# Kernel tuning notes

Measured on AMD Instinct MI355X. Metric: run time of the kernel, lower is better.

Reference implementation:

```python
import jax, jax.numpy as jnp
import numpy as np

RADIUS = 4
SIGMA_I = 10.0
SIGMA_X = 4.0
NUM_CLASSES = 8
PAD = RADIUS - 1          # 3, ConstantPad3d(radius-1, eps)
WIN = 2 * PAD + 1         # 7x7x7 window
EPS = float(np.finfo(np.float64).eps)


def _dist_flat():
    # spatial gaussian, zero outside the ball x^2+y^2+z^2 < radius^2
    r = np.arange(1 - RADIUS, RADIUS)
    xx, yy, zz = np.meshgrid(r, r, r, indexing='ij')
    d2 = (xx ** 2 + yy ** 2 + zz ** 2).astype(np.float32)
    dist = np.where(d2 < RADIUS ** 2, np.exp(-d2 / SIGMA_X ** 2), 0.0).astype(np.float32)
    return jnp.asarray(dist.reshape(-1))  # flattened x-major, matches i = x*49 + y*7 + z


def setup_inputs() -> dict:
    key = jax.random.key(0)
    k1, k2 = jax.random.split(key)
    batch = jax.random.normal(k1, (4, 1, 32, 32, 32), dtype=jnp.float32)
    preds = jax.random.uniform(k2, (4, 8, 32, 32, 32), dtype=jnp.float32)
    return {"batch": batch, "preds": preds}


def reference(batch, preds):
    B, _, D, H, W = batch.shape
    K = preds.shape[1]
    pad_cfg = ((0, 0), (0, 0), (PAD, PAD), (PAD, PAD), (PAD, PAD))
    pb = jnp.pad(batch, pad_cfg, constant_values=EPS)
    pp = jnp.pad(preds, pad_cfg, constant_values=EPS)
    dist_flat = _dist_flat()
    inv_sI2 = jnp.float32(1.0 / (SIGMA_I ** 2))

    def step(carry, i):
        numer, sumw = carry
        x = i // (WIN * WIN)
        y = (i // WIN) % WIN
        z = i % WIN
        sb = jax.lax.dynamic_slice(pb, (0, 0, x, y, z), (B, 1, D, H, W))
        sp = jax.lax.dynamic_slice(pp, (0, 0, x, y, z), (B, K, D, H, W))
        # affinity = intensity gaussian * spatial gaussian for this offset
        aff = jnp.exp(-jnp.square(batch - sb) * inv_sI2) * dist_flat[i]
        return (numer + aff * sp, sumw + aff), None

    init = (jnp.zeros((B, K, D, H, W), batch.dtype),
            jnp.zeros((B, 1, D, H, W), batch.dtype))
    (numer, sumw), _ = jax.lax.scan(step, init, jnp.arange(WIN ** 3))

    assocA = jnp.sum(numer * preds, axis=(2, 3, 4))  # (B, K)
    assocV = jnp.sum(sumw * preds, axis=(2, 3, 4))   # (B, K)
    return NUM_CLASSES - jnp.sum(assocA / assocV, axis=-1)  # (B,)
```

## Files before the change

### kernel.cpp

```cpp
#include <hip/hip_runtime.h>
#include <hip/hip_fp16.h>


#define EPS_F 2.220446049250313e-16f

constexpr int TD = 4, TH = 8, TW = 8;
constexpr int HDh = 7, HHh = 14, HWh = 14;
constexpr int SYB = 17;
constexpr int SXB = HHh * SYB;
constexpr int NB  = 6 * SXB + 13 * SYB + 13 + 1;
constexpr int NT = 512;
constexpr int NBLK = 512;
constexpr int NTASK = HDh * HHh * 4;

#define EX0 1.0f
#define EX1 0.93941306281347578611f
#define EX4 0.77880078307140486825f
#define EX9 0.56978282473092302544f

#define K1F (-0.014426950408889634f)
#define K2F (-0.09016844005556021f)

struct Ent { int off; float lw; };
struct Tab { Ent e[64]; int n; };

constexpr Tab make_tab(int half) {
    Tab t{};
    t.n = 0;
    for (int dxq = 0; dxq < 4; ++dxq)
        for (int dyi = 0; dyi < 7; ++dyi)
            for (int dzi = 0; dzi < 7; ++dzi) {
                int dy = dyi - 3, dz = dzi - 3;
                if (dxq == 0) {
                    if (dy < 0) continue;
                    if (dy == 0 && dz <= 0) continue;
                }
                int c2 = dxq * dxq + dy * dy + dz * dz;
                if (c2 >= 16) continue;
                if (((dyi + dzi) & 1) != half) continue;
                t.e[t.n].off = dxq * SXB + dy * SYB + dz;
                t.e[t.n].lw  = (float)c2 * K2F;
                ++t.n;
            }
    return t;
}
constexpr Tab TAB0 = make_tab(0);
constexpr Tab TAB1 = make_tab(1);

__device__ __forceinline__ unsigned pack2(float a, float b) {
    return (unsigned)__half_as_ushort(__float2half(a)) |
           ((unsigned)__half_as_ushort(__float2half(b)) << 16);
}

template <int HALF>
__device__ __forceinline__ void accum_pairs(const float* __restrict__ sB,
                                            const uint4* __restrict__ sPk,
                                            int vown, float b_own,
                                            float acc[9]) {
    constexpr Tab T = HALF ? TAB1 : TAB0;
    constexpr int N = HALF ? TAB1.n : TAB0.n;
    constexpr int N4 = (N / 4) * 4;

#pragma unroll
    for (int i = 0; i < N4; i += 4) {
        float sb[4];
        uint4 pk[4];
#pragma unroll
        for (int j = 0; j < 4; ++j) {
            const int nv = vown + T.e[i + j].off;
            sb[j] = sB[nv];
            pk[j] = sPk[nv];
        }
#pragma unroll
        for (int j = 0; j < 4; ++j) {
            const float d = b_own - sb[j];
            const float aff =
                __builtin_amdgcn_exp2f(__builtin_fmaf(d * d, K1F, T.e[i + j].lw));
            acc[8] += aff;
            __half2 h[4];
            __builtin_memcpy(h, &pk[j], 16);
            acc[0] = __builtin_fmaf(aff, __half2float(__low2half(h[0])),  acc[0]);
            acc[1] = __builtin_fmaf(aff, __half2float(__high2half(h[0])), acc[1]);
            acc[2] = __builtin_fmaf(aff, __half2float(__low2half(h[1])),  acc[2]);
            acc[3] = __builtin_fmaf(aff, __half2float(__high2half(h[1])), acc[3]);
            acc[4] = __builtin_fmaf(aff, __half2float(__low2half(h[2])),  acc[4]);
            acc[5] = __builtin_fmaf(aff, __half2float(__high2half(h[2])), acc[5]);
            acc[6] = __builtin_fmaf(aff, __half2float(__low2half(h[3])),  acc[6]);
            acc[7] = __builtin_fmaf(aff, __half2float(__high2half(h[3])), acc[7]);
        }
    }
#pragma unroll
    for (int i = N4; i < N; ++i) {
        const int nv = vown + T.e[i].off;
        const float sb = sB[nv];
        const uint4 pk = sPk[nv];
        const float d = b_own - sb;
        const float aff =
            __builtin_amdgcn_exp2f(__builtin_fmaf(d * d, K1F, T.e[i].lw));
        acc[8] += aff;
        __half2 h[4];
        __builtin_memcpy(h, &pk, 16);
        acc[0] = __builtin_fmaf(aff, __half2float(__low2half(h[0])),  acc[0]);
        acc[1] = __builtin_fmaf(aff, __half2float(__high2half(h[0])), acc[1]);
        acc[2] = __builtin_fmaf(aff, __half2float(__low2half(h[1])),  acc[2]);
        acc[3] = __builtin_fmaf(aff, __half2float(__high2half(h[1])), acc[3]);
        acc[4] = __builtin_fmaf(aff, __half2float(__low2half(h[2])),  acc[4]);
        acc[5] = __builtin_fmaf(aff, __half2float(__high2half(h[2])), acc[5]);
        acc[6] = __builtin_fmaf(aff, __half2float(__low2half(h[3])),  acc[6]);
        acc[7] = __builtin_fmaf(aff, __half2float(__high2half(h[3])), acc[7]);
    }
}

__global__ __launch_bounds__(NT, 4)
void softncuts_main(const float* __restrict__ batch,
                    const float* __restrict__ preds,
                    float* __restrict__ partials) {
    __shared__ float sB[NB];
    __shared__ uint4 sPk[NB];
    __shared__ float sRed[8][16];

    const int bid  = blockIdx.x;
    const int bb   = bid >> 7;
    const int tile = bid & 127;
    const int tw = tile & 3;
    const int th = (tile >> 2) & 3;
    const int td = tile >> 4;
    const int d0 = td * TD, h0 = th * TH, w0 = tw * TW;

    const int tid  = threadIdx.x;
    const int half = tid >> 8;
    const int vtid = tid & 255;
    const int lw = vtid & 7;
    const int lh = (vtid >> 3) & 7;
    const int ld = vtid >> 6;

    const float* bbase = batch + (size_t)bb * 32768;
    const float* pbase = preds + (size_t)bb * 8 * 32768;

    if (tid < NTASK) {
        const int t   = tid;
        const int c   = t & 3;
        const int row = t >> 2;
        const int hh  = row % HHh;
        const int hd  = row / HHh;
        const int gd  = d0 + hd;
        const int gh  = h0 + hh - 3;
        const int gw0 = w0 - 4 + c * 4;
        const int hwb = c * 4 - 1;
        const bool fast = (gd < 32) & ((unsigned)gh < 32u) & (gw0 >= 0) & (gw0 + 3 < 32);
        if (fast) {
            const int sidx = (gd * 32 + gh) * 32 + gw0;
            float4 pv[9];
            pv[0] = *(const float4*)(bbase + sidx);
#pragma unroll
            for (int k = 0; k < 8; ++k)
                pv[k + 1] = *(const float4*)(pbase + sidx + k * 32768);
#pragma unroll
            for (int e = 0; e < 4; ++e) {
                const int hw = hwb + e;
                if (hw < 0 || hw >= HWh) continue;
                const int f = hd * SXB + hh * SYB + hw;
                sB[f] = ((const float*)&pv[0])[e];
                unsigned u[4];
#pragma unroll
                for (int k = 0; k < 4; ++k)
                    u[k] = pack2(((const float*)&pv[2 * k + 1])[e],
                                 ((const float*)&pv[2 * k + 2])[e]);
                sPk[f] = make_uint4(u[0], u[1], u[2], u[3]);
            }
        } else {
#pragma unroll
            for (int e = 0; e < 4; ++e) {
                const int hw = hwb + e;
                if (hw < 0 || hw >= HWh) continue;
                const int gw = gw0 + e;
                const bool in = (gd < 32) & ((unsigned)gh < 32u) & ((unsigned)gw < 32u);
                const int sidx = (gd * 32 + gh) * 32 + gw;
                const int f = hd * SXB + hh * SYB + hw;
                sB[f] = in ? bbase[sidx] : EPS_F;
                unsigned u[4];
#pragma unroll
                for (int k = 0; k < 4; ++k)
                    u[k] = pack2(in ? pbase[sidx + (2 * k) * 32768]     : 0.f,
                                 in ? pbase[sidx + (2 * k + 1) * 32768] : 0.f);
                sPk[f] = make_uint4(u[0], u[1], u[2], u[3]);
            }
        }
    }
    __syncthreads();

    const int gdo = d0 + ld, gho = h0 + lh, gwo = w0 + lw;
    const int sidx_own = (gdo * 32 + gho) * 32 + gwo;
    const float b_own = bbase[sidx_own];
    float q[8];
#pragma unroll
    for (int k = 0; k < 8; ++k) q[k] = pbase[sidx_own + k * 32768];

    const int vown = ld * SXB + (lh + 3) * SYB + (lw + 3);

    float acc[9];
#pragma unroll
    for (int i = 0; i < 9; ++i) acc[i] = 0.f;

    if (half == 0) accum_pairs<0>(sB, sPk, vown, b_own, acc);
    else           accum_pairs<1>(sB, sPk, vown, b_own, acc);

    float S = 0.f;
    const bool border = (d0 < 3) | (h0 < 3) | (h0 + TH > 29) | (w0 < 3) | (w0 + TW > 29);
    if (border && half == 0) {
        constexpr float EXT[10] = {EX0, EX1, 0.f, 0.f, EX4, 0.f, 0.f, 0.f, 0.f, EX9};
        for (int dxi = 0; dxi < 7; ++dxi) {
            const int dx  = dxi - 3;
            const int dxx = dx * dx;
            const bool ind = (unsigned)(gdo + dx) < 32u;
            for (int dyi = 0; dyi < 7; ++dyi) {
                const int dy   = dyi - 3;
                const int c2xy = dxx + dy * dy;
                if (c2xy >= 16) continue;
                const float wxy = __expf((float)c2xy * -0.0625f);
                const bool inxy = ind & ((unsigned)(gho + dy) < 32u);
#pragma unroll
                for (int dzi = 0; dzi < 7; ++dzi) {
                    const int dz  = dzi - 3;
                    const int czz = dz * dz;
                    const bool neg = (dx < 0) || (dx == 0 && (dy < 0 || (dy == 0 && dz < 0)));
                    const bool valid = ((c2xy + czz) < 16) && neg;
                    const bool inall = inxy & ((unsigned)(gwo + dz) < 32u);
                    S += (valid && !inall) ? wxy * EXT[czz] : 0.f;
                }
            }
        }
    }
    const float db = b_own - EPS_F;
    const float selfpad = (half == 0) ? (1.f + S * __expf(db * db * -0.01f)) : 0.f;

    float vals[16];
#pragma unroll
    for (int k = 0; k < 8; ++k) {
        vals[k]     = q[k] * (2.f * acc[k] + ((half == 0) ? q[k] : 0.f));
        vals[8 + k] = q[k] * (acc[8] + selfpad) + acc[k];
    }

#pragma unroll
    for (int i = 0; i < 16; ++i) {
        float s = vals[i];
        for (int off = 32; off; off >>= 1) s += __shfl_down(s, off);
        vals[i] = s;
    }
    const int wave = tid >> 6;
    const int lane = tid & 63;
    if (lane == 0) {
#pragma unroll
        for (int i = 0; i < 16; ++i) sRed[wave][i] = vals[i];
    }
    __syncthreads();
    if (tid < 16) {
        float s = 0.f;
#pragma unroll
        for (int w = 0; w < 8; ++w) s += sRed[w][tid];
        partials[tid * NBLK + bid] = s;
    }
}

__global__ __launch_bounds__(1024)
void softncuts_finalize(const float* __restrict__ partials,
                        float* __restrict__ out) {
    __shared__ float red[64];
    const int tid = threadIdx.x;
    const int group = tid >> 4;
    const int j0 = tid & 15;
    const int slot = group & 15;
    const int bb = group >> 4;

    const float* p = partials + slot * NBLK + bb * 128;
    float s = 0.f;
#pragma unroll
    for (int k = 0; k < 8; ++k) s += p[j0 + 16 * k];
    for (int off = 8; off; off >>= 1) s += __shfl_down(s, off, 16);
    if (j0 == 0) red[group] = s;
    __syncthreads();

    if (tid < 4) {
        float accv = 0.f;
#pragma unroll
        for (int k = 0; k < 8; ++k)
            accv += red[tid * 16 + k] / red[tid * 16 + 8 + k];
        out[tid] = 8.0f - accv;
    }
}

extern "C" void kernel_launch(void* const* d_in, const int* in_sizes, int n_in,
                              void* d_out, int out_size, void* d_ws, size_t ws_size,
                              hipStream_t stream) {
    const float* batch = (const float*)d_in[0];
    const float* preds = (const float*)d_in[1];
    float* out      = (float*)d_out;
    float* partials = (float*)d_ws;

    softncuts_main<<<dim3(NBLK), dim3(NT), 0, stream>>>(batch, preds, partials);
    softncuts_finalize<<<dim3(1), dim3(1024), 0, stream>>>(partials, out);
}
```

Baseline: 80.85 us.

## Process two adjacent voxels per thread with union offset table and precomputed border sums

Each thread now handles two w-adjacent voxels and walks a union of both neighbour sets split four ways across thread groups. Each shared-memory neighbour load and fp16 unpack is then reused for both voxels, cutting LDS traffic per affinity. The per-thread border correction loop is replaced by a constexpr table in constant memory indexed by boundary class. The final reduction now goes through a transposed shared buffer instead of 16 wave shuffles. This costs more registers (two accumulator sets) and a larger shared allocation, which may lower occupancy.

```diff
diff --git a/kernel.cpp b/kernel.cpp
--- a/kernel.cpp
+++ b/kernel.cpp
@@ -13,80 +13,133 @@
 constexpr int NBLK = 512;
 constexpr int NTASK = HDh * HHh * 4;
 
-#define EX0 1.0f
-#define EX1 0.93941306281347578611f
-#define EX4 0.77880078307140486825f
-#define EX9 0.56978282473092302544f
-
 #define K1F (-0.014426950408889634f)
 #define K2F (-0.09016844005556021f)
 
-struct Ent { int off; float lw; };
-struct Tab { Ent e[64]; int n; };
-
-constexpr Tab make_tab(int half) {
-    Tab t{};
-    t.n = 0;
-    for (int dxq = 0; dxq < 4; ++dxq)
-        for (int dyi = 0; dyi < 7; ++dyi)
-            for (int dzi = 0; dzi < 7; ++dzi) {
-                int dy = dyi - 3, dz = dzi - 3;
-                if (dxq == 0) {
-                    if (dy < 0) continue;
-                    if (dy == 0 && dz <= 0) continue;
-                }
-                int c2 = dxq * dxq + dy * dy + dz * dz;
-                if (c2 >= 16) continue;
-                if (((dyi + dzi) & 1) != half) continue;
-                t.e[t.n].off = dxq * SXB + dy * SYB + dz;
-                t.e[t.n].lw  = (float)c2 * K2F;
+struct UEnt { int off; bool v0; bool v1; float lw0; float lw1; };
+struct UTab { UEnt e[64]; int n; };
+
+constexpr bool inH(int x, int y, int z) {
+    if (x < 0 || x > 3 || y < -3 || y > 3 || z < -3 || z > 3) return false;
+    const int c2 = x * x + y * y + z * z;
+    if (c2 == 0 || c2 >= 16) return false;
+    if (x == 0 && (y < 0 || (y == 0 && z <= 0))) return false;
+    return true;
+}
+
+constexpr UTab make_utab(int cls) {
+    UTab t{}; t.n = 0; int idx = 0;
+    for (int x = 0; x <= 3; ++x)
+        for (int y = -3; y <= 3; ++y)
+            for (int z = -3; z <= 4; ++z) {
+                const bool v0 = inH(x, y, z);
+                const bool v1 = inH(x, y, z - 1);
+                if (!v0 && !v1) continue;
+                const int my = idx & 3; ++idx;
+                if (my != cls) continue;
+                t.e[t.n].off = x * SXB + y * SYB + z;
+                t.e[t.n].v0 = v0; t.e[t.n].v1 = v1;
+                t.e[t.n].lw0 = v0 ? (float)(x * x + y * y + z * z) * K2F : 0.f;
+                t.e[t.n].lw1 = v1 ? (float)(x * x + y * y + (z - 1) * (z - 1)) * K2F : 0.f;
                 ++t.n;
             }
     return t;
 }
-constexpr Tab TAB0 = make_tab(0);
-constexpr Tab TAB1 = make_tab(1);
+constexpr UTab UT0 = make_utab(0);
+constexpr UTab UT1 = make_utab(1);
+constexpr UTab UT2 = make_utab(2);
+constexpr UTab UT3 = make_utab(3);
+
+constexpr float W16[16] = {
+    1.0f,                    0.93941306281347578611f, 0.88249690258459546286f,
+    0.82902911818040034301f, 0.77880078307140486825f, 0.73161562894664190813f,
+    0.68728927879097219970f, 0.64565423513106973593f, 0.60653065971263342360f,
+    0.56978282473092302544f, 0.53526142851899028012f, 0.50283157797094090696f,
+    0.47236655274101470713f, 0.44374731008100323837f, 0.41686201967850837523f,
+    0.39160740400665634335f };
+
+struct STab { float s[343]; };
+constexpr STab make_stab() {
+    STab t{};
+    for (int a = 0; a < 7; ++a)
+        for (int b = 0; b < 7; ++b)
+            for (int c = 0; c < 7; ++c) {
+                const int pa = a < 3 ? a : (a == 3 ? 16 : a + 25);
+                const int pb = b < 3 ? b : (b == 3 ? 16 : b + 25);
+                const int pc = c < 3 ? c : (c == 3 ? 16 : c + 25);
+                float s = 0.f;
+                for (int dx = -3; dx <= 3; ++dx)
+                    for (int dy = -3; dy <= 3; ++dy)
+                        for (int dz = -3; dz <= 3; ++dz) {
+                            const int c2 = dx * dx + dy * dy + dz * dz;
+                            if (c2 >= 16) continue;
+                            const bool neg = (dx < 0) ||
+                                (dx == 0 && (dy < 0 || (dy == 0 && dz < 0)));
+                            if (!neg) continue;
+                            const bool in = (pa + dx) >= 0 && (pa + dx) < 32 &&
+                                            (pb + dy) >= 0 && (pb + dy) < 32 &&
+                                            (pc + dz) >= 0 && (pc + dz) < 32;
+                            if (!in) s += W16[c2];
+                        }
+                t.s[(a * 7 + b) * 7 + c] = s;
+            }
+    return t;
+}
+__constant__ STab STAB = make_stab();
+
+__device__ __forceinline__ int bcls(int p) {
+    return p < 3 ? p : (p > 28 ? p - 25 : 3);
+}
 
 __device__ __forceinline__ unsigned pack2(float a, float b) {
     return (unsigned)__half_as_ushort(__float2half(a)) |
            ((unsigned)__half_as_ushort(__float2half(b)) << 16);
 }
 
-template <int HALF>
-__device__ __forceinline__ void accum_pairs(const float* __restrict__ sB,
+template <int CLS>
+__device__ __forceinline__ void accum_union(const float* __restrict__ sB,
                                             const uint4* __restrict__ sPk,
-                                            int vown, float b_own,
-                                            float acc[9]) {
-    constexpr Tab T = HALF ? TAB1 : TAB0;
-    constexpr int N = HALF ? TAB1.n : TAB0.n;
+                                            int vown, float b0, float b1,
+                                            float a0[9], float a1[9]) {
+    constexpr UTab T = CLS == 0 ? UT0 : CLS == 1 ? UT1 : CLS == 2 ? UT2 : UT3;
+    constexpr int N = T.n;
     constexpr int N4 = (N / 4) * 4;
 
 #pragma unroll
     for (int i = 0; i < N4; i += 4) {
-        float sb[4];
-        uint4 pk[4];
+        float sbv[4];
+        uint4 pkv[4];
 #pragma unroll
         for (int j = 0; j < 4; ++j) {
             const int nv = vown + T.e[i + j].off;
-            sb[j] = sB[nv];
-            pk[j] = sPk[nv];
+            sbv[j] = sB[nv];
+            pkv[j] = sPk[nv];
         }
 #pragma unroll
         for (int j = 0; j < 4; ++j) {
-            const float d = b_own - sb[j];
-            const float aff =
-                __builtin_amdgcn_exp2f(__builtin_fmaf(d * d, K1F, T.e[i + j].lw));
-            acc[8] += aff;
             __half2 h[4];
-            __builtin_memcpy(h, &pk[j], 16);
-            acc[0] = __builtin_fmaf(aff, __half2float(__low2half(h[0])),  acc[0]);
-            acc[1] = __builtin_fmaf(aff, __half2float(__high2half(h[0])), acc[1]);
-            acc[2] = __builtin_fmaf(aff, __half2float(__low2half(h[1])),  acc[2]);
-            acc[3] = __builtin_fmaf(aff, __half2float(__high2half(h[1])), acc[3]);
-            acc[4] = __builtin_fmaf(aff, __half2float(__low2half(h[2])),  acc[4]);
-            acc[5] = __builtin_fmaf(aff, __half2float(__high2half(h[2])), acc[5]);
-            acc[6] = __builtin_fmaf(aff, __half2float(__low2half(h[3])),  acc[6]);
-            acc[7] = __builtin_fmaf(aff, __half2float(__high2half(h[3])), acc[7]);
+            __builtin_memcpy(h, &pkv[j], 16);
+            float pf[8];
+            pf[0] = __half2float(__low2half(h[0]));  pf[1] = __half2float(__high2half(h[0]));
+            pf[2] = __half2float(__low2half(h[1]));  pf[3] = __half2float(__high2half(h[1]));
+            pf[4] = __half2float(__low2half(h[2]));  pf[5] = __half2float(__high2half(h[2]));
+            pf[6] = __half2float(__low2half(h[3]));  pf[7] = __half2float(__high2half(h[3]));
+            if (T.e[i + j].v0) {
+                const float d = b0 - sbv[j];
+                const float aff =
+                    __builtin_amdgcn_exp2f(__builtin_fmaf(d * d, K1F, T.e[i + j].lw0));
+                a0[8] += aff;
+#pragma unroll
+                for (int k = 0; k < 8; ++k) a0[k] = __builtin_fmaf(aff, pf[k], a0[k]);
+            }
+            if (T.e[i + j].v1) {
+                const float d = b1 - sbv[j];
+                const float aff =
+                    __builtin_amdgcn_exp2f(__builtin_fmaf(d * d, K1F, T.e[i + j].lw1));
+                a1[8] += aff;
+#pragma unroll
+                for (int k = 0; k < 8; ++k) a1[k] = __builtin_fmaf(aff, pf[k], a1[k]);
+            }
         }
     }
 #pragma unroll
@@ -94,20 +147,29 @@
         const int nv = vown + T.e[i].off;
         const float sb = sB[nv];
         const uint4 pk = sPk[nv];
-        const float d = b_own - sb;
-        const float aff =
-            __builtin_amdgcn_exp2f(__builtin_fmaf(d * d, K1F, T.e[i].lw));
-        acc[8] += aff;
         __half2 h[4];
         __builtin_memcpy(h, &pk, 16);
-        acc[0] = __builtin_fmaf(aff, __half2float(__low2half(h[0])),  acc[0]);
-        acc[1] = __builtin_fmaf(aff, __half2float(__high2half(h[0])), acc[1]);
-        acc[2] = __builtin_fmaf(aff, __half2float(__low2half(h[1])),  acc[2]);
-        acc[3] = __builtin_fmaf(aff, __half2float(__high2half(h[1])), acc[3]);
-        acc[4] = __builtin_fmaf(aff, __half2float(__low2half(h[2])),  acc[4]);
-        acc[5] = __builtin_fmaf(aff, __half2float(__high2half(h[2])), acc[5]);
-        acc[6] = __builtin_fmaf(aff, __half2float(__low2half(h[3])),  acc[6]);
-        acc[7] = __builtin_fmaf(aff, __half2float(__high2half(h[3])), acc[7]);
+        float pf[8];
+        pf[0] = __half2float(__low2half(h[0]));  pf[1] = __half2float(__high2half(h[0]));
+        pf[2] = __half2float(__low2half(h[1]));  pf[3] = __half2float(__high2half(h[1]));
+        pf[4] = __half2float(__low2half(h[2]));  pf[5] = __half2float(__high2half(h[2]));
+        pf[6] = __half2float(__low2half(h[3]));  pf[7] = __half2float(__high2half(h[3]));
+        if (T.e[i].v0) {
+            const float d = b0 - sb;
+            const float aff =
+                __builtin_amdgcn_exp2f(__builtin_fmaf(d * d, K1F, T.e[i].lw0));
+            a0[8] += aff;
+#pragma unroll
+            for (int k = 0; k < 8; ++k) a0[k] = __builtin_fmaf(aff, pf[k], a0[k]);
+        }
+        if (T.e[i].v1) {
+            const float d = b1 - sb;
+            const float aff =
+                __builtin_amdgcn_exp2f(__builtin_fmaf(d * d, K1F, T.e[i].lw1));
+            a1[8] += aff;
+#pragma unroll
+            for (int k = 0; k < 8; ++k) a1[k] = __builtin_fmaf(aff, pf[k], a1[k]);
+        }
     }
 }
 
@@ -117,7 +179,7 @@
                     float* __restrict__ partials) {
     __shared__ float sB[NB];
     __shared__ uint4 sPk[NB];
-    __shared__ float sRed[8][16];
+    __shared__ float valsT[NT * 20];
 
     const int bid  = blockIdx.x;
     const int bb   = bid >> 7;
@@ -128,11 +190,6 @@
     const int d0 = td * TD, h0 = th * TH, w0 = tw * TW;
 
     const int tid  = threadIdx.x;
-    const int half = tid >> 8;
-    const int vtid = tid & 255;
-    const int lw = vtid & 7;
-    const int lh = (vtid >> 3) & 7;
-    const int ld = vtid >> 6;
 
     const float* bbase = batch + (size_t)bb * 32768;
     const float* pbase = preds + (size_t)bb * 8 * 32768;
@@ -189,76 +246,73 @@
     }
     __syncthreads();
 
-    const int gdo = d0 + ld, gho = h0 + lh, gwo = w0 + lw;
-    const int sidx_own = (gdo * 32 + gho) * 32 + gwo;
-    const float b_own = bbase[sidx_own];
-    float q[8];
-#pragma unroll
-    for (int k = 0; k < 8; ++k) q[k] = pbase[sidx_own + k * 32768];
-
-    const int vown = ld * SXB + (lh + 3) * SYB + (lw + 3);
-
-    float acc[9];
-#pragma unroll
-    for (int i = 0; i < 9; ++i) acc[i] = 0.f;
-
-    if (half == 0) accum_pairs<0>(sB, sPk, vown, b_own, acc);
-    else           accum_pairs<1>(sB, sPk, vown, b_own, acc);
-
-    float S = 0.f;
-    const bool border = (d0 < 3) | (h0 < 3) | (h0 + TH > 29) | (w0 < 3) | (w0 + TW > 29);
-    if (border && half == 0) {
-        constexpr float EXT[10] = {EX0, EX1, 0.f, 0.f, EX4, 0.f, 0.f, 0.f, 0.f, EX9};
-        for (int dxi = 0; dxi < 7; ++dxi) {
-            const int dx  = dxi - 3;
-            const int dxx = dx * dx;
-            const bool ind = (unsigned)(gdo + dx) < 32u;
-            for (int dyi = 0; dyi < 7; ++dyi) {
-                const int dy   = dyi - 3;
-                const int c2xy = dxx + dy * dy;
-                if (c2xy >= 16) continue;
-                const float wxy = __expf((float)c2xy * -0.0625f);
-                const bool inxy = ind & ((unsigned)(gho + dy) < 32u);
-#pragma unroll
-                for (int dzi = 0; dzi < 7; ++dzi) {
-                    const int dz  = dzi - 3;
-                    const int czz = dz * dz;
-                    const bool neg = (dx < 0) || (dx == 0 && (dy < 0 || (dy == 0 && dz < 0)));
-                    const bool valid = ((c2xy + czz) < 16) && neg;
-                    const bool inall = inxy & ((unsigned)(gwo + dz) < 32u);
-                    S += (valid && !inall) ? wxy * EXT[czz] : 0.f;
-                }
-            }
-        }
-    }
-    const float db = b_own - EPS_F;
-    const float selfpad = (half == 0) ? (1.f + S * __expf(db * db * -0.01f)) : 0.f;
+    const int cid  = tid >> 7;
+    const int vtid = tid & 127;
+    const int lwp = vtid & 3;
+    const int lh  = (vtid >> 2) & 7;
+    const int ld  = vtid >> 5;
+
+    const int gdo = d0 + ld, gho = h0 + lh, gw0v = w0 + lwp * 2;
+    const int sidx0 = (gdo * 32 + gho) * 32 + gw0v;
+    const float2 bv = *(const float2*)(bbase + sidx0);
+    const float b0 = bv.x, b1 = bv.y;
+    float q0[8], q1[8];
+#pragma unroll
+    for (int k = 0; k < 8; ++k) {
+        const float2 qv = *(const float2*)(pbase + sidx0 + k * 32768);
+        q0[k] = qv.x; q1[k] = qv.y;
+    }
+
+    const int vown = ld * SXB + (lh + 3) * SYB + (lwp * 2 + 3);
+
+    float a0[9], a1[9];
+#pragma unroll
+    for (int i = 0; i < 9; ++i) { a0[i] = 0.f; a1[i] = 0.f; }
+
+    switch (cid) {
+        case 0:  accum_union<0>(sB, sPk, vown, b0, b1, a0, a1); break;
+        case 1:  accum_union<1>(sB, sPk, vown, b0, b1, a0, a1); break;
+        case 2:  accum_union<2>(sB, sPk, vown, b0, b1, a0, a1); break;
+        default: accum_union<3>(sB, sPk, vown, b0, b1, a0, a1); break;
+    }
+
+    float sp0 = 0.f, sp1 = 0.f;
+    if (cid == 0) {
+        const int base = (bcls(gdo) * 7 + bcls(gho)) * 7;
+        const float S0 = STAB.s[base + bcls(gw0v)];
+        const float S1 = STAB.s[base + bcls(gw0v + 1)];
+        const float db0 = b0 - EPS_F, db1 = b1 - EPS_F;
+        sp0 = 1.f + S0 * __expf(db0 * db0 * -0.01f);
+        sp1 = 1.f + S1 * __expf(db1 * db1 * -0.01f);
+    }
 
     float vals[16];
 #pragma unroll
     for (int k = 0; k < 8; ++k) {
-        vals[k]     = q[k] * (2.f * acc[k] + ((half == 0) ? q[k] : 0.f));
-        vals[8 + k] = q[k] * (acc[8] + selfpad) + acc[k];
-    }
-
-#pragma unroll
-    for (int i = 0; i < 16; ++i) {
-        float s = vals[i];
-        for (int off = 32; off; off >>= 1) s += __shfl_down(s, off);
-        vals[i] = s;
-    }
-    const int wave = tid >> 6;
-    const int lane = tid & 63;
-    if (lane == 0) {
-#pragma unroll
-        for (int i = 0; i < 16; ++i) sRed[wave][i] = vals[i];
+        const float s0 = (cid == 0) ? q0[k] : 0.f;
+        const float s1 = (cid == 0) ? q1[k] : 0.f;
+        vals[k]     = q0[k] * (2.f * a0[k] + s0) + q1[k] * (2.f * a1[k] + s1);
+        vals[8 + k] = q0[k] * (a0[8] + sp0) + a0[k]
+                    + q1[k] * (a1[8] + sp1) + a1[k];
+    }
+
+    {
+        float* vr = &valsT[tid * 20];
+        ((float4*)vr)[0] = make_float4(vals[0],  vals[1],  vals[2],  vals[3]);
+        ((float4*)vr)[1] = make_float4(vals[4],  vals[5],  vals[6],  vals[7]);
+        ((float4*)vr)[2] = make_float4(vals[8],  vals[9],  vals[10], vals[11]);
+        ((float4*)vr)[3] = make_float4(vals[12], vals[13], vals[14], vals[15]);
     }
     __syncthreads();
-    if (tid < 16) {
+    {
+        const int val = tid >> 5;
+        const int r   = tid & 31;
         float s = 0.f;
 #pragma unroll
-        for (int w = 0; w < 8; ++w) s += sRed[w][tid];
-        partials[tid * NBLK + bid] = s;
+        for (int k = 0; k < 16; ++k)
+            s += valsT[(r + 32 * k) * 20 + val];
+        for (int off = 16; off; off >>= 1) s += __shfl_down(s, off, 32);
+        if (r == 0) partials[val * NBLK + bid] = s;
     }
 }
 
```

Result: slower. 270.8 us (+234.9%).
